# Performance work log

Measured on AMD Instinct MI355X. Metric: run time of the kernel, lower is better.

## Reference

```python
import jax, jax.numpy as jnp
import numpy as np

B, S = 1024, 512
V, E, H, T = 50000, 300, 800, 50


def setup_inputs() -> dict:
    key = jax.random.key(0)
    ks = jax.random.split(key, 8)
    ids = jax.random.randint(ks[0], (B, S), 0, V, dtype=jnp.int64 if jax.config.jax_enable_x64 else jnp.int32)
    return {
        "ids": ids,
        "rho": jax.random.normal(ks[1], (V, E), jnp.float32) * 0.02,
        "alpha": jax.random.normal(ks[2], (T, E), jnp.float32) * 0.02,
        "W1": jax.random.normal(ks[3], (E, H), jnp.float32) * 0.05,
        "b1": jnp.zeros((H,), jnp.float32),
        "Wmu": jax.random.normal(ks[4], (H, T), jnp.float32) * 0.05,
        "bmu": jnp.zeros((T,), jnp.float32),
        "Wlv": jax.random.normal(ks[5], (H, T), jnp.float32) * 0.05,
        "blv": jnp.zeros((T,), jnp.float32),
    }


def reference(ids, rho, alpha, W1, b1, Wmu, bmu, Wlv, blv):
    b, s = ids.shape
    v = rho.shape[0]
    # bag-of-words histogram: scatter-add instead of dense one_hot+reduce_sum
    bows = jnp.zeros((b, v), rho.dtype).at[jnp.arange(b)[:, None], ids].add(1.0)
    # zero out special tokens 1 and 2 (original: x * (1 - sum(one_hot([1,2]))))
    bows = bows.at[:, jnp.array([1, 2])].set(0.0)
    normal_bows = bows / jnp.sum(bows, axis=-1, keepdims=True)
    # encoder (eval mode: dropout is identity)
    x = jnp.einsum('bv,ve->be', normal_bows, rho)
    h = jax.nn.relu(x @ W1 + b1)
    mu_theta = h @ Wmu + bmu
    logsigma_theta = h @ Wlv + blv
    kl_theta = -0.5 * jnp.sum(1.0 + logsigma_theta - mu_theta**2 - jnp.exp(logsigma_theta), axis=-1)
    # reparameterize (eval/inference mode): z = mu
    theta = jax.nn.softmax(mu_theta, axis=-1)  # [B, T]
    beta = jax.nn.softmax(jnp.einsum('te,ve->tv', alpha, rho), axis=-1)  # [T, V]
    lookup = jnp.log(theta @ beta + 1e-5)  # [B, V]
    recon_loss = -jnp.sum(lookup * bows, axis=-1)
    loss = jnp.mean(recon_loss) + jnp.mean(kl_theta)
    return theta, loss
```

## Files before the change

### kernel.cpp

```cpp
#include <hip/hip_runtime.h>
#include <math.h>


#define Bn 1024
#define Sn 512
#define Vn 50000
#define En 300
#define Hn 800
#define Tn 50
#define KP 320
#define BSTR 64
#define W1FRAG_N (50 * 10 * 64 * 8)
#define WFRAG_N  (8 * 25 * 64 * 8)
#define NRANGE 8
#define CASTB 7813
#define K4B 3128

typedef __bf16 bf16x8 __attribute__((ext_vector_type(8)));
typedef float  f32x4  __attribute__((ext_vector_type(4)));
typedef float  f32x2  __attribute__((ext_vector_type(2)));

__device__ __forceinline__ float waveReduceSum(float v) {
    #pragma unroll
    for (int off = 32; off > 0; off >>= 1) v += __shfl_xor(v, off, 64);
    return v;
}
__device__ __forceinline__ float waveReduceMax(float v) {
    #pragma unroll
    for (int off = 32; off > 0; off >>= 1) v = fmaxf(v, __shfl_xor(v, off, 64));
    return v;
}
__device__ __forceinline__ unsigned short f2bf(float x) {
    unsigned u = __float_as_uint(x);
    return (unsigned short)((u + 0x7FFFu + ((u >> 16) & 1u)) >> 16);
}
__device__ __forceinline__ float bf_lo(unsigned u) { return __uint_as_float(u << 16); }
__device__ __forceinline__ float bf_hi(unsigned u) { return __uint_as_float(u & 0xFFFF0000u); }
__device__ __forceinline__ int lane_prefix(unsigned long long m) {
    return __builtin_amdgcn_mbcnt_hi((unsigned)(m >> 32),
           __builtin_amdgcn_mbcnt_lo((unsigned)m, 0));
}
__device__ __forceinline__ void gload16a(uint4& d, const uint4* a) {
    asm volatile("global_load_dwordx4 %0, %1, off" : "=v"(d) : "v"(a));
}

#define PKACC(u) { \
    c0 += (f32x2){bf_lo((u).x), bf_hi((u).x)}; \
    c1 += (f32x2){bf_lo((u).y), bf_hi((u).y)}; \
    c2 += (f32x2){bf_lo((u).z), bf_hi((u).z)}; \
    c3 += (f32x2){bf_lo((u).w), bf_hi((u).w)}; }

__global__ __launch_bounds__(256) void ka_init(
        const float4* __restrict__ rho4, unsigned short* __restrict__ rhoh,
        const float* __restrict__ alpha, const float* __restrict__ W1,
        const float* __restrict__ Wmu, const float* __restrict__ Wlv,
        unsigned short* __restrict__ bfrag, unsigned short* __restrict__ w1frag,
        unsigned short* __restrict__ wfrag, float* __restrict__ topicsumR,
        float* __restrict__ loss) {
    if (blockIdx.x < CASTB) {
        const int i = blockIdx.x * 256 + threadIdx.x;
        if (i < Vn * (KP / 8)) {
            int v = i / (KP / 8), s8 = i - v * (KP / 8);
            int c = s8 * 8;
            ushort4 o0 = {0, 0, 0, 0}, o1 = {0, 0, 0, 0};
            if (c < En) {
                float4 r = rho4[v * (En / 4) + s8 * 2];
                o0.x = f2bf(r.x); o0.y = f2bf(r.y); o0.z = f2bf(r.z); o0.w = f2bf(r.w);
            }
            if (c + 4 < En) {
                float4 r = rho4[v * (En / 4) + s8 * 2 + 1];
                o1.x = f2bf(r.x); o1.y = f2bf(r.y); o1.z = f2bf(r.z); o1.w = f2bf(r.w);
            }
            uint4 st;
            st.x = (unsigned)o0.x | ((unsigned)o0.y << 16);
            st.y = (unsigned)o0.z | ((unsigned)o0.w << 16);
            st.z = (unsigned)o1.x | ((unsigned)o1.y << 16);
            st.w = (unsigned)o1.z | ((unsigned)o1.w << 16);
            *(uint4*)(rhoh + (size_t)v * KP + c) = st;
        }
        return;
    }
    const int gid = (blockIdx.x - CASTB) * 256 + threadIdx.x;
    if (gid < 512) topicsumR[gid] = 0.f;
    if (gid == 520) *loss = 0.f;
    if (gid < 4 * 10 * 64 * 8) {
        int j = gid & 7;
        int lane = (gid >> 3) & 63;
        int rest = gid >> 9;
        int kt = rest % 10, w = rest / 10;
        int t = 16 * w + (lane & 15);
        int e = kt * 32 + (lane >> 4) * 8 + j;
        bfrag[gid] = (t < Tn && e < En) ? f2bf(alpha[t * En + e]) : (unsigned short)0;
    }
    if (gid < W1FRAG_N) {
        int j = gid & 7, lane = (gid >> 3) & 63, rest = gid >> 9;
        int kt = rest % 10, nt = rest / 10;
        int e = kt * 32 + (lane >> 4) * 8 + j;
        int hcol = nt * 16 + (lane & 15);
        w1frag[gid] = (e < En) ? f2bf(W1[e * Hn + hcol]) : (unsigned short)0;
    } else {
        int g2 = gid - W1FRAG_N;
        if (g2 < WFRAG_N) {
            int j = g2 & 7, lane = (g2 >> 3) & 63, rest = g2 >> 9;
            int kt = rest % 25, nt = rest / 25;
            int k = kt * 32 + (lane >> 4) * 8 + j;
            int t = (nt & 3) * 16 + (lane & 15);
            float val = 0.f;
            if (t < Tn) val = (nt < 4) ? Wmu[k * Tn + t] : Wlv[k * Tn + t];
            wfrag[g2] = f2bf(val);
        }
    }
}

__global__ __launch_bounds__(256) void kb_beta_tokens(
        const unsigned short* __restrict__ rhoh,
        const unsigned short* __restrict__ bfrag,
        unsigned int* __restrict__ betaU32, float* __restrict__ topicsumR,
        const int* __restrict__ ids, int* __restrict__ toks,
        int* __restrict__ cnt, float* __restrict__ xbarP) {
    __shared__ unsigned short trans[16 * 66];
    __shared__ __align__(16) int sid[Sn];
    __shared__ int sfid[Sn];
    __shared__ __align__(16) float xred[4][320];
    __shared__ int scount, sfull;
    const int tid = threadIdx.x;
    const int wave = tid >> 6, lane = tid & 63;

    if (blockIdx.x < K4B) {
        const int x = blockIdx.x & 7;
        const int n = blockIdx.x >> 3;
        const int tile = ((x * 3125) >> 3) + n;
        if (tile >= (((x + 1) * 3125) >> 3)) return;
        const int quad = lane >> 4, l15 = lane & 15;
        const int v0 = tile * 16;
        const unsigned short* arow = rhoh + (size_t)(v0 + l15) * KP + quad * 8;
        f32x4 acc = {0.f, 0.f, 0.f, 0.f};
        #pragma unroll
        for (int kt = 0; kt < 10; ++kt) {
            bf16x8 a = *(const bf16x8*)(arow + kt * 32);
            bf16x8 bv = *(const bf16x8*)(bfrag + ((wave * 10 + kt) * 64 + lane) * 8);
            acc = __builtin_amdgcn_mfma_f32_16x16x32_bf16(a, bv, acc, 0, 0, 0);
        }
        float ts = 0.f;
        #pragma unroll
        for (int r = 0; r < 4; ++r) {
            float ev = expf(acc[r]);
            ts += ev;
            trans[(quad * 4 + r) * 66 + 16 * wave + l15] = f2bf(ev);
        }
        ts += __shfl_xor(ts, 16, 64);
        ts += __shfl_xor(ts, 32, 64);
        const int t = 16 * wave + l15;
        if (lane < 16 && t < Tn)
            atomicAdd(&topicsumR[x * 64 + t], ts);
        __syncthreads();
        unsigned int* dst = betaU32 + (size_t)v0 * 32;
        const unsigned int* tr32 = (const unsigned int*)trans;
        for (int i = tid; i < 16 * 32; i += 256)
            dst[i] = tr32[(i >> 5) * 33 + (i & 31)];
        return;
    }
    const int blk = blockIdx.x - K4B;
    const int r = blk & (NRANGE - 1), b = blk >> 3;
    const int lo = ((r * 3125) >> 3) * 16;
    const int hi = (((r + 1) * 3125) >> 3) * 16;
    if (tid == 0) { scount = 0; sfull = 0; }
    __syncthreads();
    #pragma unroll
    for (int s0 = 0; s0 < Sn; s0 += 256) {
        int id = ids[b * Sn + s0 + tid];
        bool val = (id != 1 && id != 2);
        bool inr = val && id >= lo && id < hi;
        unsigned long long mb = __ballot(inr);
        int pre = lane_prefix(mb);
        int wc = __popcll(mb);
        int base = 0;
        if (lane == 0 && wc) base = atomicAdd(&scount, wc);
        base = __shfl(base, 0, 64);
        if (inr) sid[base + pre] = id;
        if (r == 0) {
            unsigned long long fb = __ballot(val);
            int fpre = lane_prefix(fb);
            int fwc = __popcll(fb);
            int fbase = 0;
            if (lane == 0 && fwc) fbase = atomicAdd(&sfull, fwc);
            fbase = __shfl(fbase, 0, 64);
            if (val) sfid[fbase + fpre] = id;
        }
    }
    __syncthreads();
    if (r == 0) {
        const int nf = sfull;
        for (int i = tid; i < nf; i += 256) toks[b * Sn + i] = sfid[i];
        if (tid == 0) cnt[b] = nf;
    }
    const int m = scount;
    f32x2 c0 = {0.f, 0.f}, c1 = {0.f, 0.f}, c2 = {0.f, 0.f}, c3 = {0.f, 0.f};
    if (m > 0 && lane < 40) {
        const uint4* rb = (const uint4*)rhoh;
        const int mm1 = m - 1;
        uint4 A0, A1, A2, A3, B0, B1, B2, B3;
        #define ADDR(S) (rb + (size_t)sid[(S) < mm1 ? (S) : mm1] * 40 + lane)
        int s = wave;
        gload16a(A0, ADDR(s));      gload16a(A1, ADDR(s + 4));
        gload16a(A2, ADDR(s + 8));  gload16a(A3, ADDR(s + 12));
        for (;;) {
            gload16a(B0, ADDR(s + 16)); gload16a(B1, ADDR(s + 20));
            gload16a(B2, ADDR(s + 24)); gload16a(B3, ADDR(s + 28));
            asm volatile("s_waitcnt vmcnt(4)" ::: "memory");
            __builtin_amdgcn_sched_barrier(0);
            if (s < m)      PKACC(A0);
            if (s + 4 < m)  PKACC(A1);
            if (s + 8 < m)  PKACC(A2);
            if (s + 12 < m) PKACC(A3);
            s += 16;
            if (s >= m) break;
            gload16a(A0, ADDR(s + 16)); gload16a(A1, ADDR(s + 20));
            gload16a(A2, ADDR(s + 24)); gload16a(A3, ADDR(s + 28));
            asm volatile("s_waitcnt vmcnt(4)" ::: "memory");
            __builtin_amdgcn_sched_barrier(0);
            if (s < m)      PKACC(B0);
            if (s + 4 < m)  PKACC(B1);
            if (s + 8 < m)  PKACC(B2);
            if (s + 12 < m) PKACC(B3);
            s += 16;
            if (s >= m) break;
        }
        #undef ADDR
    }
    if (lane < 40) {
        float* xw = &xred[wave][lane * 8];
        *(float4*)(xw)     = (float4){c0[0], c0[1], c1[0], c1[1]};
        *(float4*)(xw + 4) = (float4){c2[0], c2[1], c3[0], c3[1]};
    }
    __syncthreads();
    float* xbp = xbarP + ((size_t)b * NRANGE + r) * KP;
    for (int c = tid; c < KP; c += 256)
        xbp[c] = xred[0][c] + xred[1][c] + xred[2][c] + xred[3][c];
}

__global__ __launch_bounds__(256) void kx_norm(
        const float* __restrict__ xbarP, const int* __restrict__ cnt,
        unsigned short* __restrict__ xsg) {
    const int i = blockIdx.x * 256 + threadIdx.x;
    const int b = i / (KP / 4), e4 = (i - b * (KP / 4)) * 4;
    const float in = 1.0f / (float)cnt[b];
    const float* bp = xbarP + ((size_t)b * NRANGE) * KP + e4;
    float sx = 0.f, sy = 0.f, sz = 0.f, sw_ = 0.f;
    #pragma unroll
    for (int rr = 0; rr < NRANGE; ++rr) {
        float4 v = *(const float4*)(bp + rr * KP);
        sx += v.x; sy += v.y; sz += v.z; sw_ += v.w;
    }
    ushort4 o;
    o.x = f2bf(sx * in); o.y = f2bf(sy * in);
    o.z = f2bf(sz * in); o.w = f2bf(sw_ * in);
    *(ushort4*)&xsg[(size_t)b * KP + e4] = o;
}

__global__ __launch_bounds__(256) void k2m_h(
        const unsigned short* __restrict__ xsg,
        const unsigned short* __restrict__ w1frag,
        const float* __restrict__ b1, unsigned short* __restrict__ hbh) {
    __shared__ unsigned short xs[16 * 328];
    const int tid = threadIdx.x;
    const int wave = tid >> 6, lane = tid & 63;
    const int quad = lane >> 4, l15 = lane & 15;
    const int b0 = blockIdx.x * 16;
    for (int i = tid; i < 16 * (KP / 8); i += 256) {
        int row = i / (KP / 8), e8 = (i - row * (KP / 8)) * 8;
        *(uint4*)&xs[row * 328 + e8] = *(const uint4*)&xsg[(size_t)(b0 + row) * KP + e8];
    }
    __syncthreads();
    const int nt = blockIdx.y * 4 + wave;
    if (nt < 50) {
        const unsigned short* arow = xs + l15 * 328 + quad * 8;
        f32x4 acc = {0.f, 0.f, 0.f, 0.f};
        #pragma unroll
        for (int kt = 0; kt < 10; ++kt) {
            bf16x8 a = *(const bf16x8*)(arow + kt * 32);
            bf16x8 bv = *(const bf16x8*)(w1frag + ((size_t)(nt * 10 + kt) * 64 + lane) * 8);
            acc = __builtin_amdgcn_mfma_f32_16x16x32_bf16(a, bv, acc, 0, 0, 0);
        }
        const int col = nt * 16 + l15;
        const float bias = b1[col];
        #pragma unroll
        for (int r = 0; r < 4; ++r) {
            int row = b0 + quad * 4 + r;
            hbh[(size_t)row * Hn + col] = f2bf(fmaxf(acc[r] + bias, 0.f));
        }
    }
}

__global__ __launch_bounds__(256) void k3_theta(
        const unsigned short* __restrict__ hbh,
        const unsigned short* __restrict__ wfrag,
        const float* __restrict__ bmu, const float* __restrict__ blv,
        float* __restrict__ theta, float* __restrict__ loss) {
    __shared__ float mlds[16 * 65];
    __shared__ float llds[16 * 65];
    const int tid = threadIdx.x;
    const int wave = tid >> 6, lane = tid & 63;
    const int quad = lane >> 4, l15 = lane & 15;
    const int b0 = blockIdx.x * 16;
    const unsigned short* arow = hbh + (size_t)(b0 + l15) * Hn + quad * 8;
    f32x4 am = {0.f, 0.f, 0.f, 0.f}, al = {0.f, 0.f, 0.f, 0.f};
    #pragma unroll
    for (int kt = 0; kt < 25; ++kt) {
        bf16x8 a  = *(const bf16x8*)(arow + kt * 32);
        bf16x8 bm = *(const bf16x8*)(wfrag + ((size_t)(wave * 25 + kt) * 64 + lane) * 8);
        bf16x8 bl = *(const bf16x8*)(wfrag + ((size_t)((4 + wave) * 25 + kt) * 64 + lane) * 8);
        am = __builtin_amdgcn_mfma_f32_16x16x32_bf16(a, bm, am, 0, 0, 0);
        al = __builtin_amdgcn_mfma_f32_16x16x32_bf16(a, bl, al, 0, 0, 0);
    }
    const int t = wave * 16 + l15;
    const float bm_ = (t < Tn) ? bmu[t] : 0.f;
    const float bl_ = (t < Tn) ? blv[t] : 0.f;
    #pragma unroll
    for (int r = 0; r < 4; ++r) {
        int row = quad * 4 + r;
        mlds[row * 65 + t] = am[r] + bm_;
        llds[row * 65 + t] = al[r] + bl_;
    }
    __syncthreads();
    const int tt = (lane < Tn) ? lane : (Tn - 1);
    const bool act = (lane < Tn);
    float klacc = 0.f;
    #pragma unroll
    for (int k = 0; k < 4; ++k) {
        int row = wave * 4 + k;
        float mu = mlds[row * 65 + tt];
        float lv = llds[row * 65 + tt];
        float m = waveReduceMax(act ? mu : -1e30f);
        float ex = act ? expf(mu - m) : 0.f;
        float ssum = waveReduceSum(ex);
        if (act) theta[(b0 + row) * Tn + lane] = ex / ssum;
        klacc += waveReduceSum(act ? (1.f + lv - mu * mu - expf(lv)) : 0.f);
    }
    if (lane == 0) atomicAdd(loss, -0.5f * klacc * (1.0f / (float)Bn));
}

__global__ __launch_bounds__(256) void k6_recon(
        const int* __restrict__ toks, const int* __restrict__ cnt,
        const float* __restrict__ theta, const float* __restrict__ topicsumR,
        const unsigned short* __restrict__ betaUh, float* __restrict__ loss) {
    __shared__ float sw[Tn];
    __shared__ float swred[4];
    const int b = blockIdx.x, tid = threadIdx.x;
    if (tid < Tn) {
        float z = 0.f;
        #pragma unroll
        for (int j = 0; j < 8; ++j) z += topicsumR[j * 64 + tid];
        sw[tid] = theta[b * Tn + tid] / z;
    }
    __syncthreads();
    float wr[Tn];
    #pragma unroll
    for (int t = 0; t < Tn; ++t) wr[t] = sw[t];
    float lsum = 0.f;
    const int n = cnt[b];
    for (int i = tid; i < n; i += 256) {
        int v = toks[b * Sn + i];
        const uint4* q = (const uint4*)(betaUh + (size_t)v * BSTR);
        float dot = 0.f;
        #pragma unroll
        for (int k = 0; k < 6; ++k) {
            uint4 u = q[k];
            int t = 8 * k;
            dot += wr[t]     * bf_lo(u.x) + wr[t + 1] * bf_hi(u.x);
            dot += wr[t + 2] * bf_lo(u.y) + wr[t + 3] * bf_hi(u.y);
            dot += wr[t + 4] * bf_lo(u.z) + wr[t + 5] * bf_hi(u.z);
            dot += wr[t + 6] * bf_lo(u.w) + wr[t + 7] * bf_hi(u.w);
        }
        unsigned d = ((const unsigned*)q)[24];
        dot += wr[48] * bf_lo(d) + wr[49] * bf_hi(d);
        lsum += logf(dot + 1e-5f);
    }
    float s = waveReduceSum(lsum);
    const int wave = tid >> 6, lane = tid & 63;
    if (lane == 0) swred[wave] = s;
    __syncthreads();
    if (tid == 0) {
        float tot = swred[0] + swred[1] + swred[2] + swred[3];
        atomicAdd(loss, -tot * (1.0f / (float)Bn));
    }
}

extern "C" void kernel_launch(void* const* d_in, const int* in_sizes, int n_in,
                              void* d_out, int out_size, void* d_ws, size_t ws_size,
                              hipStream_t stream) {
    const int*   ids   = (const int*)d_in[0];
    const float* rho   = (const float*)d_in[1];
    const float* alpha = (const float*)d_in[2];
    const float* W1    = (const float*)d_in[3];
    const float* b1    = (const float*)d_in[4];
    const float* Wmu   = (const float*)d_in[5];
    const float* bmu   = (const float*)d_in[6];
    const float* Wlv   = (const float*)d_in[7];
    const float* blv   = (const float*)d_in[8];

    float* theta = (float*)d_out;
    float* loss  = theta + Bn * Tn;

    char* w = (char*)d_ws;
    float* topicsumR = (float*)w;               w += 8 * 64 * 4;
    unsigned short* bfrag = (unsigned short*)w; w += 4 * 10 * 64 * 8 * 2;
    unsigned short* w1frag = (unsigned short*)w; w += (size_t)W1FRAG_N * 2;
    unsigned short* wfrag = (unsigned short*)w;  w += (size_t)WFRAG_N * 2;
    int*   cnt      = (int*)w;                  w += Bn * 4;
    int*   toks     = (int*)w;                  w += Bn * Sn * 4;
    float* xbarP    = (float*)w;                w += (size_t)Bn * NRANGE * KP * 4;
    unsigned short* hbh = (unsigned short*)w;   w += (size_t)Bn * Hn * 2;
    unsigned short* rhoh = (unsigned short*)w;  w += (size_t)Vn * KP * 2;
    unsigned int* betaU32 = (unsigned int*)w;   w += (size_t)Vn * 128;
    unsigned short* xsg = (unsigned short*)w;   w += (size_t)Bn * KP * 2;

    const int k0grid = (W1FRAG_N + WFRAG_N + 255) / 256;
    ka_init<<<CASTB + k0grid, 256, 0, stream>>>(
        (const float4*)rho, rhoh, alpha, W1, Wmu, Wlv,
        bfrag, w1frag, wfrag, topicsumR, loss);
    kb_beta_tokens<<<K4B + Bn * NRANGE, 256, 0, stream>>>(
        rhoh, bfrag, betaU32, topicsumR, ids, toks, cnt, xbarP);
    kx_norm<<<Bn * (KP / 4) / 256, 256, 0, stream>>>(xbarP, cnt, xsg);
    k2m_h<<<dim3(64, 13), 256, 0, stream>>>(xsg, w1frag, b1, hbh);
    k3_theta<<<64, 256, 0, stream>>>(hbh, wfrag, bmu, blv, theta, loss);
    k6_recon<<<Bn, 256, 0, stream>>>(toks, cnt, theta, topicsumR,
                                     (const unsigned short*)betaU32, loss);
}
```

Baseline: 200.0 us.

## Fuse norm, hidden and theta kernels; simplify gather loop; add nontemporal hints

Merges the x-normalization, hidden-layer GEMM and theta/KL kernels into one 64-block kernel that keeps x and h in shared memory, removing two launches and the hbh/xsg global round-trips. It also replaces the hand-pipelined inline-asm rho gather with a plain unrolled loop, and marks several streaming loads and stores as nontemporal. The fused tail runs on only 64 blocks, so the hidden GEMM loses parallelism (previously 64x13 blocks), and the simpler gather may expose more load latency.

Result: slower. 211.3 us (+5.7%).

```diff
diff --git a/kernel.cpp b/kernel.cpp
--- a/kernel.cpp
+++ b/kernel.cpp
@@ -39,9 +39,6 @@
 __device__ __forceinline__ int lane_prefix(unsigned long long m) {
     return __builtin_amdgcn_mbcnt_hi((unsigned)(m >> 32),
            __builtin_amdgcn_mbcnt_lo((unsigned)m, 0));
-}
-__device__ __forceinline__ void gload16a(uint4& d, const uint4* a) {
-    asm volatile("global_load_dwordx4 %0, %1, off" : "=v"(d) : "v"(a));
 }
 
 #define PKACC(u) { \
@@ -157,7 +154,7 @@
         unsigned int* dst = betaU32 + (size_t)v0 * 32;
         const unsigned int* tr32 = (const unsigned int*)trans;
         for (int i = tid; i < 16 * 32; i += 256)
-            dst[i] = tr32[(i >> 5) * 33 + (i & 31)];
+            __builtin_nontemporal_store(tr32[(i >> 5) * 33 + (i & 31)], &dst[i]);
         return;
     }
     const int blk = blockIdx.x - K4B;
@@ -168,7 +165,7 @@
     __syncthreads();
     #pragma unroll
     for (int s0 = 0; s0 < Sn; s0 += 256) {
-        int id = ids[b * Sn + s0 + tid];
+        int id = __builtin_nontemporal_load(&ids[b * Sn + s0 + tid]);
         bool val = (id != 1 && id != 2);
         bool inr = val && id >= lo && id < hi;
         unsigned long long mb = __ballot(inr);
@@ -191,44 +188,27 @@
     __syncthreads();
     if (r == 0) {
         const int nf = sfull;
-        for (int i = tid; i < nf; i += 256) toks[b * Sn + i] = sfid[i];
+        for (int i = tid; i < nf; i += 256)
+            __builtin_nontemporal_store(sfid[i], &toks[b * Sn + i]);
         if (tid == 0) cnt[b] = nf;
     }
     const int m = scount;
     f32x2 c0 = {0.f, 0.f}, c1 = {0.f, 0.f}, c2 = {0.f, 0.f}, c3 = {0.f, 0.f};
-    if (m > 0 && lane < 40) {
+    if (lane < 40) {
         const uint4* rb = (const uint4*)rhoh;
-        const int mm1 = m - 1;
-        uint4 A0, A1, A2, A3, B0, B1, B2, B3;
-        #define ADDR(S) (rb + (size_t)sid[(S) < mm1 ? (S) : mm1] * 40 + lane)
         int s = wave;
-        gload16a(A0, ADDR(s));      gload16a(A1, ADDR(s + 4));
-        gload16a(A2, ADDR(s + 8));  gload16a(A3, ADDR(s + 12));
-        for (;;) {
-            gload16a(B0, ADDR(s + 16)); gload16a(B1, ADDR(s + 20));
-            gload16a(B2, ADDR(s + 24)); gload16a(B3, ADDR(s + 28));
-            asm volatile("s_waitcnt vmcnt(4)" ::: "memory");
-            __builtin_amdgcn_sched_barrier(0);
-            if (s < m)      PKACC(A0);
-            if (s + 4 < m)  PKACC(A1);
-            if (s + 8 < m)  PKACC(A2);
-            if (s + 12 < m) PKACC(A3);
-            s += 16;
-            if (s >= m) break;
-            gload16a(A0, ADDR(s + 16)); gload16a(A1, ADDR(s + 20));
-            gload16a(A2, ADDR(s + 24)); gload16a(A3, ADDR(s + 28));
-            asm volatile("s_waitcnt vmcnt(4)" ::: "memory");
-            __builtin_amdgcn_sched_barrier(0);
-            if (s < m)      PKACC(B0);
-            if (s + 4 < m)  PKACC(B1);
-            if (s + 8 < m)  PKACC(B2);
-            if (s + 12 < m) PKACC(B3);
-            s += 16;
-            if (s >= m) break;
-        }
-        #undef ADDR
-    }
-    if (lane < 40) {
+        for (; s + 12 < m; s += 16) {
+            int i0 = sid[s], i1 = sid[s + 4], i2 = sid[s + 8], i3 = sid[s + 12];
+            uint4 u0 = rb[(size_t)i0 * 40 + lane];
+            uint4 u1 = rb[(size_t)i1 * 40 + lane];
+            uint4 u2 = rb[(size_t)i2 * 40 + lane];
+            uint4 u3 = rb[(size_t)i3 * 40 + lane];
+            PKACC(u0); PKACC(u1); PKACC(u2); PKACC(u3);
+        }
+        for (; s < m; s += 4) {
+            uint4 u = rb[(size_t)sid[s] * 40 + lane];
+            PKACC(u);
+        }
         float* xw = &xred[wave][lane * 8];
         *(float4*)(xw)     = (float4){c0[0], c0[1], c1[0], c1[1]};
         *(float4*)(xw + 4) = (float4){c2[0], c2[1], c3[0], c3[1]};
@@ -236,91 +216,81 @@
     __syncthreads();
     float* xbp = xbarP + ((size_t)b * NRANGE + r) * KP;
     for (int c = tid; c < KP; c += 256)
-        xbp[c] = xred[0][c] + xred[1][c] + xred[2][c] + xred[3][c];
-}
-
-__global__ __launch_bounds__(256) void kx_norm(
+        __builtin_nontemporal_store(
+            xred[0][c] + xred[1][c] + xred[2][c] + xred[3][c], &xbp[c]);
+}
+
+__global__ __launch_bounds__(256) void ktail(
         const float* __restrict__ xbarP, const int* __restrict__ cnt,
-        unsigned short* __restrict__ xsg) {
-    const int i = blockIdx.x * 256 + threadIdx.x;
-    const int b = i / (KP / 4), e4 = (i - b * (KP / 4)) * 4;
-    const float in = 1.0f / (float)cnt[b];
-    const float* bp = xbarP + ((size_t)b * NRANGE) * KP + e4;
-    float sx = 0.f, sy = 0.f, sz = 0.f, sw_ = 0.f;
-    #pragma unroll
-    for (int rr = 0; rr < NRANGE; ++rr) {
-        float4 v = *(const float4*)(bp + rr * KP);
-        sx += v.x; sy += v.y; sz += v.z; sw_ += v.w;
-    }
-    ushort4 o;
-    o.x = f2bf(sx * in); o.y = f2bf(sy * in);
-    o.z = f2bf(sz * in); o.w = f2bf(sw_ * in);
-    *(ushort4*)&xsg[(size_t)b * KP + e4] = o;
-}
-
-__global__ __launch_bounds__(256) void k2m_h(
-        const unsigned short* __restrict__ xsg,
-        const unsigned short* __restrict__ w1frag,
-        const float* __restrict__ b1, unsigned short* __restrict__ hbh) {
+        const unsigned short* __restrict__ w1frag, const float* __restrict__ b1,
+        const unsigned short* __restrict__ wfrag,
+        const float* __restrict__ bmu, const float* __restrict__ blv,
+        float* __restrict__ theta, float* __restrict__ loss) {
     __shared__ unsigned short xs[16 * 328];
+    __shared__ unsigned short hs[16 * 808];
+    __shared__ float mlds[16 * 65];
+    __shared__ float llds[16 * 65];
+    __shared__ float invn[16];
     const int tid = threadIdx.x;
     const int wave = tid >> 6, lane = tid & 63;
     const int quad = lane >> 4, l15 = lane & 15;
     const int b0 = blockIdx.x * 16;
-    for (int i = tid; i < 16 * (KP / 8); i += 256) {
-        int row = i / (KP / 8), e8 = (i - row * (KP / 8)) * 8;
-        *(uint4*)&xs[row * 328 + e8] = *(const uint4*)&xsg[(size_t)(b0 + row) * KP + e8];
-    }
-    __syncthreads();
-    const int nt = blockIdx.y * 4 + wave;
-    if (nt < 50) {
+    if (tid < 16) invn[tid] = 1.0f / (float)cnt[b0 + tid];
+    __syncthreads();
+    for (int i = tid; i < 16 * (KP / 4); i += 256) {
+        int row = i / (KP / 4), e4 = (i - row * (KP / 4)) * 4;
+        const float* bp = xbarP + ((size_t)(b0 + row) * NRANGE) * KP + e4;
+        float sx = 0.f, sy = 0.f, sz = 0.f, sw_ = 0.f;
+        #pragma unroll
+        for (int rr = 0; rr < NRANGE; ++rr) {
+            float4 v = *(const float4*)(bp + rr * KP);
+            sx += v.x; sy += v.y; sz += v.z; sw_ += v.w;
+        }
+        float in = invn[row];
+        ushort4 o;
+        o.x = f2bf(sx * in); o.y = f2bf(sy * in);
+        o.z = f2bf(sz * in); o.w = f2bf(sw_ * in);
+        *(ushort4*)&xs[row * 328 + e4] = o;
+    }
+    __syncthreads();
+    {
         const unsigned short* arow = xs + l15 * 328 + quad * 8;
-        f32x4 acc = {0.f, 0.f, 0.f, 0.f};
-        #pragma unroll
-        for (int kt = 0; kt < 10; ++kt) {
-            bf16x8 a = *(const bf16x8*)(arow + kt * 32);
-            bf16x8 bv = *(const bf16x8*)(w1frag + ((size_t)(nt * 10 + kt) * 64 + lane) * 8);
-            acc = __builtin_amdgcn_mfma_f32_16x16x32_bf16(a, bv, acc, 0, 0, 0);
-        }
-        const int col = nt * 16 + l15;
-        const float bias = b1[col];
+        for (int nt = wave; nt < 50; nt += 4) {
+            f32x4 acc = {0.f, 0.f, 0.f, 0.f};
+            #pragma unroll
+            for (int kt = 0; kt < 10; ++kt) {
+                bf16x8 a = *(const bf16x8*)(arow + kt * 32);
+                bf16x8 bv = *(const bf16x8*)(w1frag + ((size_t)(nt * 10 + kt) * 64 + lane) * 8);
+                acc = __builtin_amdgcn_mfma_f32_16x16x32_bf16(a, bv, acc, 0, 0, 0);
+            }
+            const int col = nt * 16 + l15;
+            const float bias = b1[col];
+            #pragma unroll
+            for (int r = 0; r < 4; ++r)
+                hs[(quad * 4 + r) * 808 + col] = f2bf(fmaxf(acc[r] + bias, 0.f));
+        }
+    }
+    __syncthreads();
+    {
+        const unsigned short* arow = hs + l15 * 808 + quad * 8;
+        f32x4 am = {0.f, 0.f, 0.f, 0.f}, al = {0.f, 0.f, 0.f, 0.f};
+        #pragma unroll
+        for (int kt = 0; kt < 25; ++kt) {
+            bf16x8 a  = *(const bf16x8*)(arow + kt * 32);
+            bf16x8 bm = *(const bf16x8*)(wfrag + ((size_t)(wave * 25 + kt) * 64 + lane) * 8);
+            bf16x8 bl = *(const bf16x8*)(wfrag + ((size_t)((4 + wave) * 25 + kt) * 64 + lane) * 8);
+            am = __builtin_amdgcn_mfma_f32_16x16x32_bf16(a, bm, am, 0, 0, 0);
+            al = __builtin_amdgcn_mfma_f32_16x16x32_bf16(a, bl, al, 0, 0, 0);
+        }
+        const int t = wave * 16 + l15;
+        const float bm_ = (t < Tn) ? bmu[t] : 0.f;
+        const float bl_ = (t < Tn) ? blv[t] : 0.f;
         #pragma unroll
         for (int r = 0; r < 4; ++r) {
-            int row = b0 + quad * 4 + r;
-            hbh[(size_t)row * Hn + col] = f2bf(fmaxf(acc[r] + bias, 0.f));
-        }
-    }
-}
-
-__global__ __launch_bounds__(256) void k3_theta(
-        const unsigned short* __restrict__ hbh,
-        const unsigned short* __restrict__ wfrag,
-        const float* __restrict__ bmu, const float* __restrict__ blv,
-        float* __restrict__ theta, float* __restrict__ loss) {
-    __shared__ float mlds[16 * 65];
-    __shared__ float llds[16 * 65];
-    const int tid = threadIdx.x;
-    const int wave = tid >> 6, lane = tid & 63;
-    const int quad = lane >> 4, l15 = lane & 15;
-    const int b0 = blockIdx.x * 16;
-    const unsigned short* arow = hbh + (size_t)(b0 + l15) * Hn + quad * 8;
-    f32x4 am = {0.f, 0.f, 0.f, 0.f}, al = {0.f, 0.f, 0.f, 0.f};
-    #pragma unroll
-    for (int kt = 0; kt < 25; ++kt) {
-        bf16x8 a  = *(const bf16x8*)(arow + kt * 32);
-        bf16x8 bm = *(const bf16x8*)(wfrag + ((size_t)(wave * 25 + kt) * 64 + lane) * 8);
-        bf16x8 bl = *(const bf16x8*)(wfrag + ((size_t)((4 + wave) * 25 + kt) * 64 + lane) * 8);
-        am = __builtin_amdgcn_mfma_f32_16x16x32_bf16(a, bm, am, 0, 0, 0);
-        al = __builtin_amdgcn_mfma_f32_16x16x32_bf16(a, bl, al, 0, 0, 0);
-    }
-    const int t = wave * 16 + l15;
-    const float bm_ = (t < Tn) ? bmu[t] : 0.f;
-    const float bl_ = (t < Tn) ? blv[t] : 0.f;
-    #pragma unroll
-    for (int r = 0; r < 4; ++r) {
-        int row = quad * 4 + r;
-        mlds[row * 65 + t] = am[r] + bm_;
-        llds[row * 65 + t] = al[r] + bl_;
+            int row = quad * 4 + r;
+            mlds[row * 65 + t] = am[r] + bm_;
+            llds[row * 65 + t] = al[r] + bl_;
+        }
     }
     __syncthreads();
     const int tt = (lane < Tn) ? lane : (Tn - 1);
@@ -410,10 +380,8 @@
     int*   cnt      = (int*)w;                  w += Bn * 4;
     int*   toks     = (int*)w;                  w += Bn * Sn * 4;
     float* xbarP    = (float*)w;                w += (size_t)Bn * NRANGE * KP * 4;
-    unsigned short* hbh = (unsigned short*)w;   w += (size_t)Bn * Hn * 2;
     unsigned short* rhoh = (unsigned short*)w;  w += (size_t)Vn * KP * 2;
     unsigned int* betaU32 = (unsigned int*)w;   w += (size_t)Vn * 128;
-    unsigned short* xsg = (unsigned short*)w;   w += (size_t)Bn * KP * 2;
 
     const int k0grid = (W1FRAG_N + WFRAG_N + 255) / 256;
     ka_init<<<CASTB + k0grid, 256, 0, stream>>>(
@@ -421,9 +389,8 @@
         bfrag, w1frag, wfrag, topicsumR, loss);
     kb_beta_tokens<<<K4B + Bn * NRANGE, 256, 0, stream>>>(
         rhoh, bfrag, betaU32, topicsumR, ids, toks, cnt, xbarP);
-    kx_norm<<<Bn * (KP / 4) / 256, 256, 0, stream>>>(xbarP, cnt, xsg);
-    k2m_h<<<dim3(64, 13), 256, 0, stream>>>(xsg, w1frag, b1, hbh);
-    k3_theta<<<64, 256, 0, stream>>>(hbh, wfrag, bmu, blv, theta, loss);
+    ktail<<<64, 256, 0, stream>>>(xbarP, cnt, w1frag, b1, wfrag, bmu, blv,
+                                  theta, loss);
     k6_recon<<<Bn, 256, 0, stream>>>(toks, cnt, theta, topicsumR,
                                      (const unsigned short*)betaU32, loss);
 }
```
